# Kernel tuning notes

Measured on AMD Instinct MI355X. Metric: run time of the kernel, lower is better.

## Reference

```python
import jax, jax.numpy as jnp
import numpy as np

N_HEADS = 4
N_GROUPS = 32
EPS = 1e-5


def setup_inputs() -> dict:
    key = jax.random.key(0)
    ks = jax.random.split(key, 6)
    c = 512
    x = jax.random.normal(ks[0], (4, c, 64, 64), dtype=jnp.float32)
    # conv1x1 weights ~ kaiming-ish scale
    s = 1.0 / np.sqrt(c)
    wq = jax.random.normal(ks[1], (c, c), dtype=jnp.float32) * s
    wk = jax.random.normal(ks[2], (c, c), dtype=jnp.float32) * s
    wv = jax.random.normal(ks[3], (c, c), dtype=jnp.float32) * s
    wp = jax.random.normal(ks[4], (c, c), dtype=jnp.float32) * s
    zeros = jnp.zeros((c,), dtype=jnp.float32)
    return {
        "x": x,
        "gn_w": jnp.ones((c,), dtype=jnp.float32), "gn_b": zeros,
        "wq": wq, "bq": zeros, "wk": wk, "bk": zeros,
        "wv": wv, "bv": zeros, "wp": wp, "bp": zeros,
    }


def _group_norm(x, w, b):
    bsz, c, h, wd = x.shape
    xg = x.reshape(bsz, N_GROUPS, c // N_GROUPS, h, wd)
    mean = xg.mean(axis=(2, 3, 4), keepdims=True)
    var = xg.var(axis=(2, 3, 4), keepdims=True)
    xg = (xg - mean) * jax.lax.rsqrt(var + EPS)
    x = xg.reshape(bsz, c, h, wd)
    return x * w[None, :, None, None] + b[None, :, None, None]


def _conv1x1(x, w, b):
    # x: (b,c,h,w), w: (out,in) -> (b,out,h,w)
    return jnp.einsum('bchw,oc->bohw', x, w) + b[None, :, None, None]


def reference(x, gn_w, gn_b, wq, bq, wk, bk, wv, bv, wp, bp):
    bsz, c, h, wd = x.shape
    hd = c // N_HEADS
    hw = h * wd
    x_n = _group_norm(x, gn_w, gn_b)
    q = _conv1x1(x_n, wq, bq)
    k = _conv1x1(x_n, wk, bk)
    v = _conv1x1(x_n, wv, bv)

    def to_heads(t):
        # (b,c,h,w) -> (b, n_heads, hw, head_dim)
        return t.reshape(bsz, N_HEADS, hd, hw).transpose(0, 1, 3, 2)

    q, k, v = to_heads(q), to_heads(k), to_heads(v)
    scale = hd ** (-0.5)
    attn = jnp.einsum('bhqd,bhkd->bhqk', q, k) * scale  # (b,H,hw,hw)
    attn = jax.nn.softmax(attn, axis=-1)
    out = jnp.einsum('bhqk,bhkd->bhqd', attn, v)
    out = out.transpose(0, 1, 3, 2).reshape(bsz, c, h, wd)
    out = _conv1x1(out, wp, bp)
    return x + out
```

## Files before the change

### kernel.cpp

```cpp
#include <hip/hip_runtime.h>
#include <math.h>

typedef __attribute__((ext_vector_type(8))) short short8;
typedef __attribute__((ext_vector_type(4))) float floatx4;
typedef __attribute__((ext_vector_type(16))) float floatx16;
typedef __attribute__((ext_vector_type(8))) unsigned short ushort8v;
typedef __attribute__((ext_vector_type(4))) unsigned short ushort4v;

#define HW 4096
#define CCH 512
#define NB 4
#define NH 4
#define HD 128

__device__ __forceinline__ unsigned short f2bf(float f) {
    union { float f; unsigned int u; } c; c.f = f;
    unsigned int u = c.u;
    u += 0x7FFFu + ((u >> 16) & 1u);
    return (unsigned short)(u >> 16);
}

__device__ __forceinline__ void gload_lds16(const unsigned short* g, unsigned short* l) {
    __builtin_amdgcn_global_load_lds(
        (const __attribute__((address_space(1))) unsigned int*)g,
        (__attribute__((address_space(3))) unsigned int*)l, 16, 0, 0);
}

__global__ void conv_w(const float* __restrict__ w0, const float* __restrict__ w1,
                       const float* __restrict__ w2, const float* __restrict__ w3,
                       unsigned short* __restrict__ dst) {
    const float* src = blockIdx.y == 0 ? w0 : blockIdx.y == 1 ? w1 : blockIdx.y == 2 ? w2 : w3;
    unsigned short* d = dst + (size_t)blockIdx.y * 262144;
    int i = blockIdx.x * 256 + threadIdx.x;
    float4 v = ((const float4*)src)[i];
    ushort4v o;
    o[0] = f2bf(v.x); o[1] = f2bf(v.y); o[2] = f2bf(v.z); o[3] = f2bf(v.w);
    ((ushort4v*)d)[i] = o;
}

__global__ void gn_stats(const float* __restrict__ x, float* __restrict__ stats) {
    int bg = blockIdx.x;
    int b = bg >> 5, g = bg & 31;
    const float4* p = (const float4*)(x + ((size_t)b * CCH + g * 16) * HW);
    float s = 0.f, ss = 0.f;
    for (int i = threadIdx.x; i < 16384; i += 256) {
        float4 v = p[i];
        s  += v.x + v.y + v.z + v.w;
        ss += v.x * v.x + v.y * v.y + v.z * v.z + v.w * v.w;
    }
    #pragma unroll
    for (int off = 32; off > 0; off >>= 1) {
        s  += __shfl_down(s, off, 64);
        ss += __shfl_down(ss, off, 64);
    }
    __shared__ float sm[4], sm2[4];
    int wid = threadIdx.x >> 6;
    if ((threadIdx.x & 63) == 0) { sm[wid] = s; sm2[wid] = ss; }
    __syncthreads();
    if (threadIdx.x == 0) {
        float ts = sm[0] + sm[1] + sm[2] + sm[3];
        float tss = sm2[0] + sm2[1] + sm2[2] + sm2[3];
        float mean = ts * (1.f / 65536.f);
        float var = tss * (1.f / 65536.f) - mean * mean;
        stats[bg * 2] = mean;
        stats[bg * 2 + 1] = rsqrtf(var + 1e-5f);
    }
}

__global__ void gn_apply(const float* __restrict__ x, const float* __restrict__ gnw,
                         const float* __restrict__ gnb, const float* __restrict__ stats,
                         unsigned short* __restrict__ xt) {
    int s = blockIdx.x * 256 + threadIdx.x;
    int g = blockIdx.y, b = blockIdx.z;
    float mean = stats[(b * 32 + g) * 2];
    float rstd = stats[(b * 32 + g) * 2 + 1];
    const float* xb = x + ((size_t)b * CCH + g * 16) * HW + s;
    unsigned short outv[16];
    #pragma unroll
    for (int cl = 0; cl < 16; cl++) {
        int c = g * 16 + cl;
        float v = xb[(size_t)cl * HW];
        v = (v - mean) * rstd * gnw[c] + gnb[c];
        outv[cl] = f2bf(v);
    }
    unsigned short* dst = xt + ((size_t)b * HW + s) * CCH + g * 16;
    *(ushort8v*)dst       = *(ushort8v*)&outv[0];
    *(ushort8v*)(dst + 8) = *(ushort8v*)&outv[8];
}

#define LDP 72
template <int MODE>
__global__ __launch_bounds__(256, 2) void gemm_nt(
    const unsigned short* __restrict__ A, long long aStride,
    const unsigned short* __restrict__ Bm, long long bStride,
    const float* __restrict__ bias, float scale,
    const float* __restrict__ resid, long long rStride,
    void* __restrict__ Cp, long long cStride, int ldc) {
    __shared__ unsigned short lA[2][128 * LDP];
    __shared__ unsigned short lB[2][128 * LDP];
    const int tid = threadIdx.x;
    const int lane = tid & 63;
    const int wid = tid >> 6;
    const int z = blockIdx.z;
    const unsigned short* Ab = A + (size_t)z * aStride + (size_t)blockIdx.x * 128 * 512;
    const unsigned short* Bb = Bm + (size_t)z * bStride + (size_t)blockIdx.y * 128 * 512;

    floatx4 acc[4][4];
    #pragma unroll
    for (int i = 0; i < 4; i++)
        #pragma unroll
        for (int j = 0; j < 4; j++) acc[i][j] = (floatx4)0.f;

    const int wm = (wid >> 1) * 64;
    const int wn = (wid & 1) * 64;
    const int l15 = lane & 15;
    const int l4 = lane >> 4;
    const int srow = tid >> 3;
    const int skc  = (tid & 7) * 8;

    ushort8v ar[4], br[4];
    #pragma unroll
    for (int i = 0; i < 4; i++) {
        int row = srow + i * 32;
        ar[i] = *(const ushort8v*)&Ab[(size_t)row * 512 + skc];
        br[i] = *(const ushort8v*)&Bb[(size_t)row * 512 + skc];
    }
    #pragma unroll
    for (int i = 0; i < 4; i++) {
        int row = srow + i * 32;
        *(ushort8v*)&lA[0][row * LDP + skc] = ar[i];
        *(ushort8v*)&lB[0][row * LDP + skc] = br[i];
    }
    __syncthreads();

    int cur = 0;
    #pragma unroll 1
    for (int t = 0; t < 8; t++) {
        if (t < 7) {
            int k0 = (t + 1) * 64;
            #pragma unroll
            for (int i = 0; i < 4; i++) {
                int row = srow + i * 32;
                ar[i] = *(const ushort8v*)&Ab[(size_t)row * 512 + k0 + skc];
                br[i] = *(const ushort8v*)&Bb[(size_t)row * 512 + k0 + skc];
            }
        }
        #pragma unroll
        for (int kk = 0; kk < 2; kk++) {
            short8 af[4], bf[4];
            #pragma unroll
            for (int i = 0; i < 4; i++)
                af[i] = *(const short8*)&lA[cur][(wm + i * 16 + l15) * LDP + kk * 32 + l4 * 8];
            #pragma unroll
            for (int j = 0; j < 4; j++)
                bf[j] = *(const short8*)&lB[cur][(wn + j * 16 + l15) * LDP + kk * 32 + l4 * 8];
            #pragma unroll
            for (int i = 0; i < 4; i++)
                #pragma unroll
                for (int j = 0; j < 4; j++)
                    acc[i][j] = __builtin_amdgcn_mfma_f32_16x16x32_bf16(af[i], bf[j], acc[i][j], 0, 0, 0);
        }
        if (t < 7) {
            int nxt = cur ^ 1;
            #pragma unroll
            for (int i = 0; i < 4; i++) {
                int row = srow + i * 32;
                *(ushort8v*)&lA[nxt][row * LDP + skc] = ar[i];
                *(ushort8v*)&lB[nxt][row * LDP + skc] = br[i];
            }
            __syncthreads();
            cur = nxt;
        }
    }

    long long m0 = (long long)blockIdx.x * 128 + wm;
    long long n0 = (long long)blockIdx.y * 128 + wn;
    if (MODE == 0 || MODE == 3) {
        unsigned short* C = (unsigned short*)Cp + (size_t)z * cStride;
        const float* bptr = (MODE == 3 && z == 1) ? resid : bias;
        float sc = (MODE == 3 && z == 1) ? 1.f : scale;
        #pragma unroll
        for (int i = 0; i < 4; i++)
            #pragma unroll
            for (int j = 0; j < 4; j++) {
                long long col = n0 + j * 16 + l15;
                float bv = bptr[col];
                #pragma unroll
                for (int r = 0; r < 4; r++) {
                    long long row = m0 + i * 16 + l4 * 4 + r;
                    C[row * ldc + col] = f2bf((acc[i][j][r] + bv) * sc);
                }
            }
    } else if (MODE == 1) {
        float* C = (float*)Cp + (size_t)z * cStride;
        const float* R = resid + (size_t)z * rStride;
        #pragma unroll
        for (int i = 0; i < 4; i++)
            #pragma unroll
            for (int j = 0; j < 4; j++)
                #pragma unroll
                for (int r = 0; r < 4; r++) {
                    long long row = m0 + i * 16 + l4 * 4 + r;
                    long long col = n0 + j * 16 + l15;
                    C[row * ldc + col] = acc[i][j][r] + bias[row] + R[row * ldc + col];
                }
    } else {
        unsigned short* C = (unsigned short*)Cp + (size_t)z * cStride;
        #pragma unroll
        for (int i = 0; i < 4; i++)
            #pragma unroll
            for (int j = 0; j < 4; j++)
                #pragma unroll
                for (int r = 0; r < 4; r++) {
                    long long row = m0 + i * 16 + l4 * 4 + r;
                    long long col = n0 + j * 16 + l15;
                    C[row * ldc + col] = f2bf(acc[i][j][r] + bias[row]);
                }
    }
}

__global__ __launch_bounds__(256, 2) void attn_kern(
    const unsigned short* __restrict__ Qb, const unsigned short* __restrict__ Kb,
    const unsigned short* __restrict__ Vt, unsigned short* __restrict__ Ob) {
    __shared__ __align__(16) unsigned short lk0[8192], lk1[8192];
    __shared__ __align__(16) unsigned short lv0[8192], lv1[8192];
    const int tid = threadIdx.x;
    const int lane = tid & 63;
    const int w = tid >> 6;
    const int l31 = lane & 31;
    const int l1 = lane >> 5;
    const int q0 = blockIdx.x * 128;
    const int h = blockIdx.y, b = blockIdx.z;
    const size_t headOff = (size_t)h * HD;
    const size_t batchRow = (size_t)b * HW;
    const unsigned short* VtB = Vt + ((size_t)b * CCH + headOff) * HW;

    size_t kSrc[4], vSrc[4];
    #pragma unroll
    for (int n = 0; n < 4; n++) {
        int row = w * 16 + n * 4 + (lane >> 4);
        int sk = ((row & 7) << 1) | ((row >> 3) & 1);
        int jk = (lane & 15) ^ sk;
        kSrc[n] = (batchRow + row) * 512 + headOff + jk * 8;
        int d = w * 32 + n * 8 + (lane >> 3);
        int jv = (lane & 7) ^ (d & 7);
        vSrc[n] = (size_t)d * HW + jv * 8;
    }
    const int ldsOff = w * 4 * 512;

    const int sk0 = ((l31 & 7) << 1) | ((l31 >> 3) & 1);
    const int sv0 = l31 & 7;

    short8 qf[8];
    #pragma unroll
    for (int kd = 0; kd < 8; kd++)
        qf[kd] = *(const short8*)&Qb[(batchRow + q0 + w * 32 + l31) * 512
                                     + headOff + kd * 16 + l1 * 8];

    short8 onesf;
    #pragma unroll
    for (int e = 0; e < 8; e++) onesf[e] = (short)0x3F80;

    floatx16 acc_o[4];
    floatx16 acc_l;
    acc_l = (floatx16)0.f;
    #pragma unroll
    for (int dj = 0; dj < 4; dj++) acc_o[dj] = (floatx16)0.f;

    #pragma unroll
    for (int n = 0; n < 4; n++) gload_lds16(&Kb[kSrc[n]], lk0 + ldsOff + n * 512);
    #pragma unroll
    for (int n = 0; n < 4; n++) gload_lds16(&Kb[kSrc[n] + (size_t)64 * 512], lk1 + ldsOff + n * 512);
    #pragma unroll
    for (int n = 0; n < 4; n++) gload_lds16(&VtB[vSrc[n]], lv0 + ldsOff + n * 512);
    __syncthreads();

    floatx16 sa0 = (floatx16)0.f, sa1 = (floatx16)0.f;
    #pragma unroll
    for (int kd = 0; kd < 8; kd++) {
        int xk = ((kd * 2 + l1) ^ sk0) * 8;
        short8 kf0 = *(const short8*)&lk0[l31 * 128 + xk];
        short8 kf1 = *(const short8*)&lk0[l31 * 128 + xk + 4096];
        sa0 = __builtin_amdgcn_mfma_f32_32x32x16_bf16(kf0, qf[kd], sa0, 0, 0, 0);
        sa1 = __builtin_amdgcn_mfma_f32_32x32x16_bf16(kf1, qf[kd], sa1, 0, 0, 0);
    }
    __syncthreads();

    unsigned short* lvCur = lv0;  unsigned short* lvNxt = lv1;
    unsigned short* kRead = lk1;  unsigned short* kWrite = lk0;

    #pragma unroll 1
    for (int kt = 0; kt < 63; kt++) {
        {
            size_t tv = (size_t)(kt + 1) * 64;
            size_t tk = (size_t)(kt + 2) * 64 * 512;
            #pragma unroll
            for (int n = 0; n < 4; n++) gload_lds16(&VtB[vSrc[n] + tv], lvNxt + ldsOff + n * 512);
            #pragma unroll
            for (int n = 0; n < 4; n++) gload_lds16(&Kb[kSrc[n] + tk], kWrite + ldsOff + n * 512);
        }

        short8 paf[4];
        #pragma unroll
        for (int r = 0; r < 16; r++) sa0[r] = __builtin_amdgcn_exp2f(sa0[r]);
        #pragma unroll
        for (int r = 0; r < 16; r++) sa1[r] = __builtin_amdgcn_exp2f(sa1[r]);
        #pragma unroll
        for (int tb = 0; tb < 2; tb++) {
            const floatx16& sa = tb ? sa1 : sa0;
            unsigned int wv[4][2];
            #pragma unroll
            for (int g = 0; g < 4; g++) {
                asm("v_cvt_pk_bf16_f32 %0, %1, %2" : "=v"(wv[g][0])
                    : "v"(sa[4 * g + 0]), "v"(sa[4 * g + 1]));
                asm("v_cvt_pk_bf16_f32 %0, %1, %2" : "=v"(wv[g][1])
                    : "v"(sa[4 * g + 2]), "v"(sa[4 * g + 3]));
            }
            #pragma unroll
            for (int hh = 0; hh < 2; hh++) {
                unsigned int a0 = wv[2 * hh][0], b0 = wv[2 * hh + 1][0];
                unsigned int a1 = wv[2 * hh][1], b1 = wv[2 * hh + 1][1];
                asm("v_permlane32_swap_b32 %0, %1" : "+v"(a0), "+v"(b0));
                asm("v_permlane32_swap_b32 %0, %1" : "+v"(a1), "+v"(b1));
                union { unsigned int u[4]; short8 s8; } f;
                f.u[0] = a0; f.u[1] = a1; f.u[2] = b0; f.u[3] = b1;
                paf[2 * tb + hh] = f.s8;
            }
        }

        sa0 = (floatx16)0.f; sa1 = (floatx16)0.f;
        __builtin_amdgcn_s_setprio(1);
        #pragma unroll
        for (int u = 0; u < 4; u++) {
            #pragma unroll
            for (int q2 = 0; q2 < 2; q2++) {
                int kd = u * 2 + q2;
                int xk = ((kd * 2 + l1) ^ sk0) * 8;
                short8 kf0 = *(const short8*)&kRead[l31 * 128 + xk];
                short8 kf1 = *(const short8*)&kRead[l31 * 128 + xk + 4096];
                sa0 = __builtin_amdgcn_mfma_f32_32x32x16_bf16(kf0, qf[kd], sa0, 0, 0, 0);
                sa1 = __builtin_amdgcn_mfma_f32_32x32x16_bf16(kf1, qf[kd], sa1, 0, 0, 0);
            }
            acc_l = __builtin_amdgcn_mfma_f32_32x32x16_bf16(paf[u], onesf, acc_l, 0, 0, 0);
            int xv = ((u * 2 + l1) ^ sv0) * 8;
            #pragma unroll
            for (int dj = 0; dj < 4; dj++) {
                short8 vv = *(const short8*)&lvCur[dj * 2048 + l31 * 64 + xv];
                acc_o[dj] = __builtin_amdgcn_mfma_f32_32x32x16_bf16(paf[u], vv, acc_o[dj], 0, 0, 0);
            }
        }
        __builtin_amdgcn_s_setprio(0);

        __syncthreads();
        unsigned short* t;
        t = lvCur; lvCur = lvNxt; lvNxt = t;
        t = kRead; kRead = kWrite; kWrite = t;
    }

    {
        short8 paf[4];
        #pragma unroll
        for (int r = 0; r < 16; r++) sa0[r] = __builtin_amdgcn_exp2f(sa0[r]);
        #pragma unroll
        for (int r = 0; r < 16; r++) sa1[r] = __builtin_amdgcn_exp2f(sa1[r]);
        #pragma unroll
        for (int tb = 0; tb < 2; tb++) {
            const floatx16& sa = tb ? sa1 : sa0;
            unsigned int wv[4][2];
            #pragma unroll
            for (int g = 0; g < 4; g++) {
                asm("v_cvt_pk_bf16_f32 %0, %1, %2" : "=v"(wv[g][0])
                    : "v"(sa[4 * g + 0]), "v"(sa[4 * g + 1]));
                asm("v_cvt_pk_bf16_f32 %0, %1, %2" : "=v"(wv[g][1])
                    : "v"(sa[4 * g + 2]), "v"(sa[4 * g + 3]));
            }
            #pragma unroll
            for (int hh = 0; hh < 2; hh++) {
                unsigned int a0 = wv[2 * hh][0], b0 = wv[2 * hh + 1][0];
                unsigned int a1 = wv[2 * hh][1], b1 = wv[2 * hh + 1][1];
                asm("v_permlane32_swap_b32 %0, %1" : "+v"(a0), "+v"(b0));
                asm("v_permlane32_swap_b32 %0, %1" : "+v"(a1), "+v"(b1));
                union { unsigned int u[4]; short8 s8; } f;
                f.u[0] = a0; f.u[1] = a1; f.u[2] = b0; f.u[3] = b1;
                paf[2 * tb + hh] = f.s8;
            }
        }
        __builtin_amdgcn_s_setprio(1);
        #pragma unroll
        for (int u = 0; u < 4; u++) {
            acc_l = __builtin_amdgcn_mfma_f32_32x32x16_bf16(paf[u], onesf, acc_l, 0, 0, 0);
            int xv = ((u * 2 + l1) ^ sv0) * 8;
            #pragma unroll
            for (int dj = 0; dj < 4; dj++) {
                short8 vv = *(const short8*)&lvCur[dj * 2048 + l31 * 64 + xv];
                acc_o[dj] = __builtin_amdgcn_mfma_f32_32x32x16_bf16(paf[u], vv, acc_o[dj], 0, 0, 0);
            }
        }
        __builtin_amdgcn_s_setprio(0);
    }

    #pragma unroll
    for (int g = 0; g < 4; g++)
        #pragma unroll
        for (int p = 0; p < 4; p++) {
            int reg = 4 * g + p;
            float rl = 1.f / acc_l[reg];
            int qr = p + 8 * g + 4 * l1;
            size_t row = batchRow + q0 + w * 32 + qr;
            #pragma unroll
            for (int dj = 0; dj < 4; dj++)
                Ob[row * 512 + headOff + dj * 32 + l31] = f2bf(acc_o[dj][reg] * rl);
        }
}

extern "C" void kernel_launch(void* const* d_in, const int* in_sizes, int n_in,
                              void* d_out, int out_size, void* d_ws, size_t ws_size,
                              hipStream_t stream) {
    const float* x   = (const float*)d_in[0];
    const float* gnw = (const float*)d_in[1];
    const float* gnb = (const float*)d_in[2];
    const float* wq  = (const float*)d_in[3];
    const float* bq  = (const float*)d_in[4];
    const float* wk  = (const float*)d_in[5];
    const float* bk  = (const float*)d_in[6];
    const float* wv  = (const float*)d_in[7];
    const float* bv  = (const float*)d_in[8];
    const float* wp  = (const float*)d_in[9];
    const float* bp  = (const float*)d_in[10];
    float* out = (float*)d_out;

    const size_t NE = (size_t)NB * HW * CCH;
    unsigned short* ws16 = (unsigned short*)d_ws;
    unsigned short* XT = ws16;
    unsigned short* Qb = ws16 + NE;
    unsigned short* Kb = ws16 + 2 * NE;
    unsigned short* Vt = ws16 + 3 * NE;
    unsigned short* Wb = ws16 + 4 * NE;
    float* stats = (float*)(ws16 + 4 * NE + 4 * 262144);

    const float qscale = 0.08838834764831845f * 1.4426950408889634f;

    conv_w<<<dim3(256, 4), 256, 0, stream>>>(wq, wk, wv, wp, Wb);
    gn_stats<<<128, 256, 0, stream>>>(x, stats);
    gn_apply<<<dim3(16, 32, 4), 256, 0, stream>>>(x, gnw, gnb, stats, XT);

    gemm_nt<3><<<dim3(128, 4, 2), 256, 0, stream>>>(XT, 0, Wb, 262144, bq, qscale, bk, 0,
                                                    Qb, (long long)NE, 512);
    gemm_nt<2><<<dim3(4, 32, 4), 256, 0, stream>>>(Wb + 2 * 262144, 0, XT, (long long)HW * 512, bv, 1.f,
                                                   nullptr, 0, Vt, (long long)CCH * HW, HW);

    unsigned short* Ob = XT;
    attn_kern<<<dim3(32, NH, NB), 256, 0, stream>>>(Qb, Kb, Vt, Ob);

    gemm_nt<1><<<dim3(4, 32, 4), 256, 0, stream>>>(Wb + 3 * 262144, 0, Ob, (long long)HW * 512, bp, 1.f,
                                                   x, (long long)CCH * HW, out, (long long)CCH * HW, HW);
}
```

Baseline: 332.8 us.

## Software-pipeline QK and PV across tiles, replace ones-MFMA row sum with VALU

Restructures the attention main loop into a two-stage software pipeline. Each step computes S for the next K tile into a ping-pong register set while the exp, pack and PV MFMAs run on the previous tile's scores, manually unrolled by two to avoid register copies. It also drops the extra MFMA against a ones matrix used for the softmax denominator. Instead each lane sums its fp32 exponentials, combines halves with a permlane32 swap, and broadcasts per row with a shuffle in the epilogue. This removes one MFMA per sub-tile and exposes more overlap between matrix and vector work, at the cost of extra VGPRs for the second score buffer and VALU adds. The denominator is now summed from fp32 values rather than bf16-rounded ones.

Result: no change. 336.9 us (+1.2%).

```diff
diff --git a/kernel.cpp b/kernel.cpp
--- a/kernel.cpp
+++ b/kernel.cpp
@@ -24,6 +24,11 @@
     __builtin_amdgcn_global_load_lds(
         (const __attribute__((address_space(1))) unsigned int*)g,
         (__attribute__((address_space(3))) unsigned int*)l, 16, 0, 0);
+}
+
+__device__ __forceinline__ float sum16(const floatx16& s) {
+    return ((((s[0] + s[1]) + (s[2] + s[3])) + ((s[4] + s[5]) + (s[6] + s[7])))
+          + (((s[8] + s[9]) + (s[10] + s[11])) + ((s[12] + s[13]) + (s[14] + s[15]))));
 }
 
 __global__ void conv_w(const float* __restrict__ w0, const float* __restrict__ w1,
@@ -257,15 +262,10 @@
         qf[kd] = *(const short8*)&Qb[(batchRow + q0 + w * 32 + l31) * 512
                                      + headOff + kd * 16 + l1 * 8];
 
-    short8 onesf;
-    #pragma unroll
-    for (int e = 0; e < 8; e++) onesf[e] = (short)0x3F80;
-
     floatx16 acc_o[4];
-    floatx16 acc_l;
-    acc_l = (floatx16)0.f;
     #pragma unroll
     for (int dj = 0; dj < 4; dj++) acc_o[dj] = (floatx16)0.f;
+    float lsum_part = 0.f;
 
     #pragma unroll
     for (int n = 0; n < 4; n++) gload_lds16(&Kb[kSrc[n]], lk0 + ldsOff + n * 512);
@@ -275,39 +275,31 @@
     for (int n = 0; n < 4; n++) gload_lds16(&VtB[vSrc[n]], lv0 + ldsOff + n * 512);
     __syncthreads();
 
-    floatx16 sa0 = (floatx16)0.f, sa1 = (floatx16)0.f;
+    floatx16 saA0 = (floatx16)0.f, saA1 = (floatx16)0.f;
+    floatx16 saB0, saB1;
     #pragma unroll
     for (int kd = 0; kd < 8; kd++) {
         int xk = ((kd * 2 + l1) ^ sk0) * 8;
         short8 kf0 = *(const short8*)&lk0[l31 * 128 + xk];
         short8 kf1 = *(const short8*)&lk0[l31 * 128 + xk + 4096];
-        sa0 = __builtin_amdgcn_mfma_f32_32x32x16_bf16(kf0, qf[kd], sa0, 0, 0, 0);
-        sa1 = __builtin_amdgcn_mfma_f32_32x32x16_bf16(kf1, qf[kd], sa1, 0, 0, 0);
+        saA0 = __builtin_amdgcn_mfma_f32_32x32x16_bf16(kf0, qf[kd], saA0, 0, 0, 0);
+        saA1 = __builtin_amdgcn_mfma_f32_32x32x16_bf16(kf1, qf[kd], saA1, 0, 0, 0);
     }
     __syncthreads();
 
     unsigned short* lvCur = lv0;  unsigned short* lvNxt = lv1;
     unsigned short* kRead = lk1;  unsigned short* kWrite = lk0;
 
-    #pragma unroll 1
-    for (int kt = 0; kt < 63; kt++) {
-        {
-            size_t tv = (size_t)(kt + 1) * 64;
-            size_t tk = (size_t)(kt + 2) * 64 * 512;
-            #pragma unroll
-            for (int n = 0; n < 4; n++) gload_lds16(&VtB[vSrc[n] + tv], lvNxt + ldsOff + n * 512);
-            #pragma unroll
-            for (int n = 0; n < 4; n++) gload_lds16(&Kb[kSrc[n] + tk], kWrite + ldsOff + n * 512);
-        }
-
+    auto pack_pv = [&](floatx16& s0, floatx16& s1) {
+        #pragma unroll
+        for (int r = 0; r < 16; r++) s0[r] = __builtin_amdgcn_exp2f(s0[r]);
+        #pragma unroll
+        for (int r = 0; r < 16; r++) s1[r] = __builtin_amdgcn_exp2f(s1[r]);
+        lsum_part += sum16(s0) + sum16(s1);
         short8 paf[4];
         #pragma unroll
-        for (int r = 0; r < 16; r++) sa0[r] = __builtin_amdgcn_exp2f(sa0[r]);
-        #pragma unroll
-        for (int r = 0; r < 16; r++) sa1[r] = __builtin_amdgcn_exp2f(sa1[r]);
-        #pragma unroll
         for (int tb = 0; tb < 2; tb++) {
-            const floatx16& sa = tb ? sa1 : sa0;
+            const floatx16& sa = tb ? s1 : s0;
             unsigned int wv[4][2];
             #pragma unroll
             for (int g = 0; g < 4; g++) {
@@ -327,21 +319,8 @@
                 paf[2 * tb + hh] = f.s8;
             }
         }
-
-        sa0 = (floatx16)0.f; sa1 = (floatx16)0.f;
-        __builtin_amdgcn_s_setprio(1);
         #pragma unroll
         for (int u = 0; u < 4; u++) {
-            #pragma unroll
-            for (int q2 = 0; q2 < 2; q2++) {
-                int kd = u * 2 + q2;
-                int xk = ((kd * 2 + l1) ^ sk0) * 8;
-                short8 kf0 = *(const short8*)&kRead[l31 * 128 + xk];
-                short8 kf1 = *(const short8*)&kRead[l31 * 128 + xk + 4096];
-                sa0 = __builtin_amdgcn_mfma_f32_32x32x16_bf16(kf0, qf[kd], sa0, 0, 0, 0);
-                sa1 = __builtin_amdgcn_mfma_f32_32x32x16_bf16(kf1, qf[kd], sa1, 0, 0, 0);
-            }
-            acc_l = __builtin_amdgcn_mfma_f32_32x32x16_bf16(paf[u], onesf, acc_l, 0, 0, 0);
             int xv = ((u * 2 + l1) ^ sv0) * 8;
             #pragma unroll
             for (int dj = 0; dj < 4; dj++) {
@@ -349,54 +328,49 @@
                 acc_o[dj] = __builtin_amdgcn_mfma_f32_32x32x16_bf16(paf[u], vv, acc_o[dj], 0, 0, 0);
             }
         }
+    };
+
+    auto step = [&](int kt, floatx16& sO0, floatx16& sO1, floatx16& sN0, floatx16& sN1) {
+        size_t tv = (size_t)(kt + 1) * 64;
+        size_t tk = (size_t)(kt + 2) * 64 * 512;
+        #pragma unroll
+        for (int n = 0; n < 4; n++) gload_lds16(&VtB[vSrc[n] + tv], lvNxt + ldsOff + n * 512);
+        #pragma unroll
+        for (int n = 0; n < 4; n++) gload_lds16(&Kb[kSrc[n] + tk], kWrite + ldsOff + n * 512);
+
+        sN0 = (floatx16)0.f; sN1 = (floatx16)0.f;
+        __builtin_amdgcn_s_setprio(1);
+        #pragma unroll
+        for (int kd = 0; kd < 8; kd++) {
+            int xk = ((kd * 2 + l1) ^ sk0) * 8;
+            short8 kf0 = *(const short8*)&kRead[l31 * 128 + xk];
+            short8 kf1 = *(const short8*)&kRead[l31 * 128 + xk + 4096];
+            sN0 = __builtin_amdgcn_mfma_f32_32x32x16_bf16(kf0, qf[kd], sN0, 0, 0, 0);
+            sN1 = __builtin_amdgcn_mfma_f32_32x32x16_bf16(kf1, qf[kd], sN1, 0, 0, 0);
+        }
+        pack_pv(sO0, sO1);
         __builtin_amdgcn_s_setprio(0);
 
         __syncthreads();
-        unsigned short* t;
-        t = lvCur; lvCur = lvNxt; lvNxt = t;
-        t = kRead; kRead = kWrite; kWrite = t;
-    }
-
+        unsigned short* t_;
+        t_ = lvCur; lvCur = lvNxt; lvNxt = t_;
+        t_ = kRead; kRead = kWrite; kWrite = t_;
+    };
+
+    #pragma unroll 1
+    for (int it = 0; it < 31; it++) {
+        step(2 * it,     saA0, saA1, saB0, saB1);
+        step(2 * it + 1, saB0, saB1, saA0, saA1);
+    }
+    step(62, saA0, saA1, saB0, saB1);
+    pack_pv(saB0, saB1);
+
+    float tot;
     {
-        short8 paf[4];
-        #pragma unroll
-        for (int r = 0; r < 16; r++) sa0[r] = __builtin_amdgcn_exp2f(sa0[r]);
-        #pragma unroll
-        for (int r = 0; r < 16; r++) sa1[r] = __builtin_amdgcn_exp2f(sa1[r]);
-        #pragma unroll
-        for (int tb = 0; tb < 2; tb++) {
-            const floatx16& sa = tb ? sa1 : sa0;
-            unsigned int wv[4][2];
-            #pragma unroll
-            for (int g = 0; g < 4; g++) {
-                asm("v_cvt_pk_bf16_f32 %0, %1, %2" : "=v"(wv[g][0])
-                    : "v"(sa[4 * g + 0]), "v"(sa[4 * g + 1]));
-                asm("v_cvt_pk_bf16_f32 %0, %1, %2" : "=v"(wv[g][1])
-                    : "v"(sa[4 * g + 2]), "v"(sa[4 * g + 3]));
-            }
-            #pragma unroll
-            for (int hh = 0; hh < 2; hh++) {
-                unsigned int a0 = wv[2 * hh][0], b0 = wv[2 * hh + 1][0];
-                unsigned int a1 = wv[2 * hh][1], b1 = wv[2 * hh + 1][1];
-                asm("v_permlane32_swap_b32 %0, %1" : "+v"(a0), "+v"(b0));
-                asm("v_permlane32_swap_b32 %0, %1" : "+v"(a1), "+v"(b1));
-                union { unsigned int u[4]; short8 s8; } f;
-                f.u[0] = a0; f.u[1] = a1; f.u[2] = b0; f.u[3] = b1;
-                paf[2 * tb + hh] = f.s8;
-            }
-        }
-        __builtin_amdgcn_s_setprio(1);
-        #pragma unroll
-        for (int u = 0; u < 4; u++) {
-            acc_l = __builtin_amdgcn_mfma_f32_32x32x16_bf16(paf[u], onesf, acc_l, 0, 0, 0);
-            int xv = ((u * 2 + l1) ^ sv0) * 8;
-            #pragma unroll
-            for (int dj = 0; dj < 4; dj++) {
-                short8 vv = *(const short8*)&lvCur[dj * 2048 + l31 * 64 + xv];
-                acc_o[dj] = __builtin_amdgcn_mfma_f32_32x32x16_bf16(paf[u], vv, acc_o[dj], 0, 0, 0);
-            }
-        }
-        __builtin_amdgcn_s_setprio(0);
+        union { float f; unsigned int u; } ua, ub;
+        ua.f = lsum_part; ub.f = lsum_part;
+        asm("v_permlane32_swap_b32 %0, %1" : "+v"(ua.u), "+v"(ub.u));
+        tot = ua.f + ub.f;
     }
 
     #pragma unroll
@@ -404,8 +378,8 @@
         #pragma unroll
         for (int p = 0; p < 4; p++) {
             int reg = 4 * g + p;
-            float rl = 1.f / acc_l[reg];
             int qr = p + 8 * g + 4 * l1;
+            float rl = 1.f / __shfl(tot, qr, 64);
             size_t row = batchRow + q0 + w * 32 + qr;
             #pragma unroll
             for (int dj = 0; dj < 4; dj++)
```

## Load GEMM tiles directly to LDS with XOR-swizzled single buffer

Applied to the files above, without the earlier changes.

Replaces the register-staged, double-buffered, padded LDS tile loads in gemm_nt with direct global_load_lds transfers into a single unpadded LDS buffer that uses an XOR swizzle to avoid bank conflicts. LDS use is halved and launch bounds are raised to allow 3 blocks per CU. The cost is losing the prefetch overlap: each k-step now issues its loads, waits on a barrier, computes, then barriers again, so global latency is exposed unless higher occupancy hides it.

New measurement: 336.0 us. Within noise of the previous version (+1.0%).

```diff
diff --git a/kernel.cpp b/kernel.cpp
--- a/kernel.cpp
+++ b/kernel.cpp
@@ -88,16 +88,15 @@
     *(ushort8v*)(dst + 8) = *(ushort8v*)&outv[8];
 }
 
-#define LDP 72
 template <int MODE>
-__global__ __launch_bounds__(256, 2) void gemm_nt(
+__global__ __launch_bounds__(256, 3) void gemm_nt(
     const unsigned short* __restrict__ A, long long aStride,
     const unsigned short* __restrict__ Bm, long long bStride,
     const float* __restrict__ bias, float scale,
     const float* __restrict__ resid, long long rStride,
     void* __restrict__ Cp, long long cStride, int ldc) {
-    __shared__ unsigned short lA[2][128 * LDP];
-    __shared__ unsigned short lB[2][128 * LDP];
+    __shared__ __align__(16) unsigned short lA[128 * 64];
+    __shared__ __align__(16) unsigned short lB[128 * 64];
     const int tid = threadIdx.x;
     const int lane = tid & 63;
     const int wid = tid >> 6;
@@ -115,62 +114,42 @@
     const int wn = (wid & 1) * 64;
     const int l15 = lane & 15;
     const int l4 = lane >> 4;
-    const int srow = tid >> 3;
-    const int skc  = (tid & 7) * 8;
-
-    ushort8v ar[4], br[4];
-    #pragma unroll
-    for (int i = 0; i < 4; i++) {
-        int row = srow + i * 32;
-        ar[i] = *(const ushort8v*)&Ab[(size_t)row * 512 + skc];
-        br[i] = *(const ushort8v*)&Bb[(size_t)row * 512 + skc];
-    }
-    #pragma unroll
-    for (int i = 0; i < 4; i++) {
-        int row = srow + i * 32;
-        *(ushort8v*)&lA[0][row * LDP + skc] = ar[i];
-        *(ushort8v*)&lB[0][row * LDP + skc] = br[i];
-    }
-    __syncthreads();
-
-    int cur = 0;
+    const int sxr = l15 & 7;
+
+    size_t srcOff[4];
+    int dstBase[4];
+    #pragma unroll
+    for (int n = 0; n < 4; n++) {
+        int row = n * 32 + (tid >> 3);
+        int g = tid & 7;
+        srcOff[n] = (size_t)row * 512 + (size_t)((g ^ (row & 7)) << 3);
+        dstBase[n] = (n * 256 + wid * 64) * 8;
+    }
+
     #pragma unroll 1
     for (int t = 0; t < 8; t++) {
-        if (t < 7) {
-            int k0 = (t + 1) * 64;
-            #pragma unroll
-            for (int i = 0; i < 4; i++) {
-                int row = srow + i * 32;
-                ar[i] = *(const ushort8v*)&Ab[(size_t)row * 512 + k0 + skc];
-                br[i] = *(const ushort8v*)&Bb[(size_t)row * 512 + k0 + skc];
-            }
-        }
+        int k0 = t * 64;
+        #pragma unroll
+        for (int n = 0; n < 4; n++) gload_lds16(&Ab[srcOff[n] + k0], lA + dstBase[n]);
+        #pragma unroll
+        for (int n = 0; n < 4; n++) gload_lds16(&Bb[srcOff[n] + k0], lB + dstBase[n]);
+        __syncthreads();
         #pragma unroll
         for (int kk = 0; kk < 2; kk++) {
             short8 af[4], bf[4];
             #pragma unroll
             for (int i = 0; i < 4; i++)
-                af[i] = *(const short8*)&lA[cur][(wm + i * 16 + l15) * LDP + kk * 32 + l4 * 8];
+                af[i] = *(const short8*)&lA[(wm + i * 16 + l15) * 64 + (((kk * 4 + l4) ^ sxr) << 3)];
             #pragma unroll
             for (int j = 0; j < 4; j++)
-                bf[j] = *(const short8*)&lB[cur][(wn + j * 16 + l15) * LDP + kk * 32 + l4 * 8];
+                bf[j] = *(const short8*)&lB[(wn + j * 16 + l15) * 64 + (((kk * 4 + l4) ^ sxr) << 3)];
             #pragma unroll
             for (int i = 0; i < 4; i++)
                 #pragma unroll
                 for (int j = 0; j < 4; j++)
                     acc[i][j] = __builtin_amdgcn_mfma_f32_16x16x32_bf16(af[i], bf[j], acc[i][j], 0, 0, 0);
         }
-        if (t < 7) {
-            int nxt = cur ^ 1;
-            #pragma unroll
-            for (int i = 0; i < 4; i++) {
-                int row = srow + i * 32;
-                *(ushort8v*)&lA[nxt][row * LDP + skc] = ar[i];
-                *(ushort8v*)&lB[nxt][row * LDP + skc] = br[i];
-            }
-            __syncthreads();
-            cur = nxt;
-        }
+        if (t < 7) __syncthreads();
     }
 
     long long m0 = (long long)blockIdx.x * 128 + wm;
```
